# Performance work log

Hardware: AMD Instinct MI355X
Metric: run time of the kernel (lower is better)

## Reference

```python
import jax, jax.numpy as jnp
import numpy as np

N, T, V, C, H = 16, 512, 33, 3, 64
EPS = 1e-5
CONNECTIONS = [(0,1),(1,2),(2,3),(3,7),(0,4),(4,5),(5,6),(6,8),(9,10),(11,12),(11,13),(13,15),(12,14),(14,16),(15,17),(15,19),(15,21),(17,19),(16,18),(16,20),(16,22),(18,20),(11,23),(12,24),(23,24),(23,25),(25,27),(24,26),(26,28),(27,29),(27,31),(29,31),(28,30),(28,32)]


def _adjacency():
    A = np.zeros((V, V), dtype=np.float32)
    for i, j in CONNECTIONS:
        A[i, j] = 1.0
        A[j, i] = 1.0
    A = A + np.eye(V, dtype=np.float32)
    return jnp.asarray(A / A.sum(axis=1, keepdims=True))  # D^{-1} A row-normalization


def setup_inputs() -> dict:
    key = jax.random.key(0)
    ks = iter(jax.random.split(key, 80))
    def nrm(shape, s=0.05):
        return jax.random.normal(next(ks), shape, jnp.float32) * s
    d = {"x": jax.random.normal(next(ks), (N, T, V, C), jnp.float32), "A": _adjacency()}
    def bn(prefix, shape):
        d[prefix + "g"] = 1.0 + nrm(shape, 0.1)
        d[prefix + "b"] = nrm(shape, 0.1)
        d[prefix + "m"] = jnp.zeros(shape, jnp.float32)
        d[prefix + "v"] = jnp.ones(shape, jnp.float32)
    bn("dbn_", (C * V,))
    d["b1_gw"] = nrm((H, C)); d["b1_gb"] = nrm((H,))
    bn("b1_bn1", (H,)); d["b1_tw"] = nrm((H, H, 9)); d["b1_tb"] = nrm((H,)); bn("b1_bn2", (H,))
    d["m_gw"] = nrm((3, H, H)); d["m_gb"] = nrm((3, H))
    bn("m_bn1", (3, H)); d["m_tw"] = nrm((3, H, H, 9)); d["m_tb"] = nrm((3, H)); bn("m_bn2", (3, H))
    d["b5_gw"] = nrm((C, H)); d["b5_gb"] = nrm((C,))
    bn("b5_bn1", (C,)); d["b5_tw"] = nrm((C, C, 9)); d["b5_tb"] = nrm((C,)); bn("b5_bn2", (C,))
    return d


def _bn2d(y, g, b, m, v):
    sh = (1, -1, 1, 1)
    return (y - m.reshape(sh)) * (g.reshape(sh) * jax.lax.rsqrt(v.reshape(sh) + EPS)) + b.reshape(sh)


def _block(y, A, gw, gb, g1, b1, m1, v1, tw, tb, g2, b2, m2, v2, residual):
    res = y if residual else 0.0
    # GraphConv: 1x1 conv (K=1 partition) then joint aggregation with normalized adjacency
    z = jnp.einsum('nctv,oc->notv', y, gw) + gb.reshape(1, -1, 1, 1)
    z = jnp.einsum('nctv,vw->nctw', z, A)
    # TCN: BN -> ReLU -> 9x1 temporal conv (pad 4) -> BN (dropout identity in eval)
    z = jax.nn.relu(_bn2d(z, g1, b1, m1, v1))
    z = jax.lax.conv_general_dilated(z, tw[..., None], (1, 1), [(4, 4), (0, 0)],
                                     dimension_numbers=('NCHW', 'OIHW', 'NCHW')) + tb.reshape(1, -1, 1, 1)
    z = _bn2d(z, g2, b2, m2, v2)
    return jax.nn.relu(z + res)


def _forward(x, A, dbn_g, dbn_b, dbn_m, dbn_v, b1_gw, b1_gb, b1_bn1g, b1_bn1b, b1_bn1m, b1_bn1v, b1_tw, b1_tb, b1_bn2g, b1_bn2b, b1_bn2m, b1_bn2v, m_gw, m_gb, m_bn1g, m_bn1b, m_bn1m, m_bn1v, m_tw, m_tb, m_bn2g, m_bn2b, m_bn2m, m_bn2v, b5_gw, b5_gb, b5_bn1g, b5_bn1b, b5_bn1m, b5_bn1v, b5_tw, b5_tb, b5_bn2g, b5_bn2b, b5_bn2m, b5_bn2v):
    xc = jnp.transpose(x, (0, 3, 1, 2))  # N,C,T,V
    # data_bn: raw view of NCTV contiguous buffer as (N, C*V, T), matching torch .view
    xr = xc.reshape(N, C * V, T)
    xr = (xr - dbn_m[:, None]) * (dbn_g[:, None] * jax.lax.rsqrt(dbn_v[:, None] + EPS)) + dbn_b[:, None]
    y = xr.reshape(N, C, T, V)
    y = _block(y, A, b1_gw, b1_gb, b1_bn1g, b1_bn1b, b1_bn1m, b1_bn1v, b1_tw, b1_tb, b1_bn2g, b1_bn2b, b1_bn2m, b1_bn2v, False)
    for i in range(3):
        y = _block(y, A, m_gw[i], m_gb[i], m_bn1g[i], m_bn1b[i], m_bn1m[i], m_bn1v[i], m_tw[i], m_tb[i], m_bn2g[i], m_bn2b[i], m_bn2m[i], m_bn2v[i], True)
    y = _block(y, A, b5_gw, b5_gb, b5_bn1g, b5_bn1b, b5_bn1m, b5_bn1v, b5_tw, b5_tb, b5_bn2g, b5_bn2b, b5_bn2m, b5_bn2v, False)
    return jnp.transpose(xc + y, (0, 2, 3, 1))  # N,T,V,C


def reference(x, A, dbn_g, dbn_b, dbn_m, dbn_v, b1_gw, b1_gb, b1_bn1g, b1_bn1b, b1_bn1m, b1_bn1v, b1_tw, b1_tb, b1_bn2g, b1_bn2b, b1_bn2m, b1_bn2v, m_gw, m_gb, m_bn1g, m_bn1b, m_bn1m, m_bn1v, m_tw, m_tb, m_bn2g, m_bn2b, m_bn2m, m_bn2v, b5_gw, b5_gb, b5_bn1g, b5_bn1b, b5_bn1m, b5_bn1v, b5_tw, b5_tb, b5_bn2g, b5_bn2b, b5_bn2m, b5_bn2v):
    return _forward(x, A, dbn_g, dbn_b, dbn_m, dbn_v, b1_gw, b1_gb, b1_bn1g, b1_bn1b, b1_bn1m, b1_bn1v, b1_tw, b1_tb, b1_bn2g, b1_bn2b, b1_bn2m, b1_bn2v, m_gw, m_gb, m_bn1g, m_bn1b, m_bn1m, m_bn1v, m_tw, m_tb, m_bn2g, m_bn2b, m_bn2m, m_bn2v, b5_gw, b5_gb, b5_bn1g, b5_bn1b, b5_bn1m, b5_bn1v, b5_tw, b5_tb, b5_bn2g, b5_bn2b, b5_bn2m, b5_bn2v)
```

## Files before the change

kernel.cpp:

```cpp
#include <hip/hip_runtime.h>
#include <hip/hip_bf16.h>


constexpr int N_ = 16, T_ = 512, V_ = 33, C_ = 3, H_ = 64;
constexpr float EPS_ = 1e-5f;

typedef __attribute__((ext_vector_type(8))) short short8;
typedef __attribute__((ext_vector_type(4))) float f32x4;

__device__ inline unsigned short f2bf(float f) {
    union { __hip_bfloat16 h; unsigned short u; } cv;
    cv.h = __float2bfloat16(f);
    return cv.u;
}
__device__ inline float bf2f(unsigned short u) {
    union { unsigned short u; __hip_bfloat16 h; } cv;
    cv.u = u;
    return __bfloat162float(cv.h);
}

__global__ __launch_bounds__(256) void k_prep(
    const float* __restrict__ b1_tw, const float* __restrict__ m_tw,
    const float* __restrict__ b1_gw, const float* __restrict__ m_gw,
    const float* __restrict__ Adj,
    unsigned short* __restrict__ wT_bf, unsigned short* __restrict__ gw_bf,
    unsigned short* __restrict__ ATbf, float* __restrict__ colsum,
    float* __restrict__ gwT_b1)
{
    int idx = blockIdx.x * 256 + threadIdx.x;
    if (idx < 147456) {
        int s = idx / 36864, r = idx % 36864;
        int k = r / 4096, o = (r % 4096) / 64, i = r % 64;
        const float* src = (s == 0) ? b1_tw : (m_tw + (size_t)(s - 1) * 36864);
        wT_bf[idx] = f2bf(src[(o * 64 + i) * 9 + k]);
    } else if (idx < 147456 + 12288) {
        int r = idx - 147456;
        gw_bf[r] = f2bf(m_gw[r]);
    } else if (idx < 147456 + 12288 + 3456) {
        int r = idx - 159744;
        int w = r / 72, vv = r % 72;
        ATbf[r] = (w < 33 && vv < 33) ? f2bf(Adj[vv * 33 + w]) : (unsigned short)0;
    } else if (idx < 147456 + 12288 + 3456 + 48) {
        int w = idx - 163200;
        float s = 0.f;
        if (w < 33)
            for (int vv = 0; vv < 33; ++vv) s += Adj[vv * 33 + w];
        colsum[w] = s;
    } else if (idx < 147456 + 12288 + 3456 + 48 + 192) {
        int r = idx - 163248;
        int c = r / 64, o = r % 64;
        gwT_b1[r] = b1_gw[o * 3 + c];
    }
}

__global__ __launch_bounds__(256) void k_stageA_b1(
    const float* __restrict__ x,
    unsigned short* __restrict__ out,
    const float* __restrict__ Adj,
    const float* __restrict__ gwT,
    const float* __restrict__ gb,
    const float* __restrict__ g1, const float* __restrict__ b1,
    const float* __restrict__ m1, const float* __restrict__ v1,
    const float* __restrict__ dg, const float* __restrict__ db,
    const float* __restrict__ dm, const float* __restrict__ dv)
{
    __shared__ float sy[V_ * 4];
    __shared__ float su[V_ * 68];
    __shared__ float sA[V_ * V_];
    __shared__ float sgwT[3 * 64];

    int nt = blockIdx.x;
    int t = nt & (T_ - 1);
    int tid = threadIdx.x;
    const float* src = x + (size_t)nt * (V_ * 3);
    for (int idx = tid; idx < V_ * 3; idx += 256) {
        int v = idx / 3, c = idx % 3;
        int jj = c * V_ + ((t * V_ + v) >> 9);
        float s = dg[jj] * rsqrtf(dv[jj] + EPS_);
        sy[v * 4 + c] = (src[idx] - dm[jj]) * s + db[jj];
    }
    for (int idx = tid; idx < V_ * V_; idx += 256) sA[idx] = Adj[idx];
    for (int idx = tid; idx < 3 * 64; idx += 256) sgwT[idx] = gwT[idx];
    __syncthreads();

    for (int idx = tid; idx < V_ * 16; idx += 256) {
        int v = idx >> 4, oq = idx & 15, o4 = oq * 4;
        float a0 = gb[o4], a1 = gb[o4 + 1], a2 = gb[o4 + 2], a3 = gb[o4 + 3];
#pragma unroll
        for (int c = 0; c < 3; ++c) {
            float yv = sy[v * 4 + c];
            const float4 w4 = *reinterpret_cast<const float4*>(&sgwT[c * 64 + o4]);
            a0 = fmaf(yv, w4.x, a0); a1 = fmaf(yv, w4.y, a1);
            a2 = fmaf(yv, w4.z, a2); a3 = fmaf(yv, w4.w, a3);
        }
        *reinterpret_cast<float4*>(&su[v * 68 + o4]) = make_float4(a0, a1, a2, a3);
    }
    __syncthreads();

    for (int idx = tid; idx < V_ * 16; idx += 256) {
        int w = idx >> 4, oq = idx & 15, o4 = oq * 4;
        float a0 = 0.f, a1 = 0.f, a2 = 0.f, a3 = 0.f;
        for (int v = 0; v < V_; ++v) {
            float av = sA[v * V_ + w];
            const float4 u4 = *reinterpret_cast<const float4*>(&su[v * 68 + o4]);
            a0 = fmaf(av, u4.x, a0); a1 = fmaf(av, u4.y, a1);
            a2 = fmaf(av, u4.z, a2); a3 = fmaf(av, u4.w, a3);
        }
        float acc[4] = {a0, a1, a2, a3};
        unsigned short r4[4];
#pragma unroll
        for (int j = 0; j < 4; ++j) {
            int o = o4 + j;
            float s = g1[o] * rsqrtf(v1[o] + EPS_);
            float tt = b1[o] - m1[o] * s;
            r4[j] = f2bf(fmaxf(fmaf(acc[j], s, tt), 0.f));
        }
        *reinterpret_cast<ushort4*>(&out[(size_t)nt * (V_ * 64) + w * 64 + o4]) =
            *reinterpret_cast<ushort4*>(r4);
    }
}

__global__ __launch_bounds__(256) void k_stageA_mfma(
    const unsigned short* __restrict__ in,
    unsigned short* __restrict__ out,
    const unsigned short* __restrict__ ATbf,
    const float* __restrict__ colsum,
    const unsigned short* __restrict__ gwbf,
    const float* __restrict__ gb,
    const float* __restrict__ g1, const float* __restrict__ b1,
    const float* __restrict__ m1, const float* __restrict__ v1)
{
    __shared__ unsigned short Ys[4 * 48 * 72];
    __shared__ unsigned short UT[64 * 72];
    __shared__ float cs[48];

    int nt0 = blockIdx.x * 4;
    int tid = threadIdx.x;
    int wv = tid >> 6, lane = tid & 63;
    int l15 = lane & 15, lg = lane >> 4;
    int o = wv * 16 + l15;

    short8 atf[3][2];
#pragma unroll
    for (int mf = 0; mf < 3; ++mf)
#pragma unroll
        for (int kk = 0; kk < 2; ++kk)
            atf[mf][kk] = *reinterpret_cast<const short8*>(
                ATbf + (16 * mf + l15) * 72 + kk * 32 + lg * 8);
    short8 gwf[2];
#pragma unroll
    for (int kk = 0; kk < 2; ++kk)
        gwf[kk] = *reinterpret_cast<const short8*>(gwbf + o * 64 + kk * 32 + lg * 8);

    float gbl = gb[o];
    float s1 = g1[o] * rsqrtf(v1[o] + EPS_);
    float c1 = b1[o] - m1[o] * s1;

    for (int idx = tid; idx < 1056; idx += 256) {
        int j = idx / 264, r = idx % 264;
        int v = r >> 3, cc = r & 7;
        *reinterpret_cast<short8*>(&Ys[(j * 48 + v) * 72 + cc * 8]) =
            *reinterpret_cast<const short8*>(in + ((size_t)(nt0 + j) * V_ + v) * 64 + cc * 8);
    }
    for (int idx = tid; idx < 540; idx += 256) {
        int j = idx / 135, r = idx % 135;
        int v = 33 + r / 9, cc = r % 9;
        short8 z = {};
        *reinterpret_cast<short8*>(&Ys[(j * 48 + v) * 72 + cc * 8]) = z;
    }
    for (int idx = tid; idx < 128; idx += 256) {
        int oo = idx >> 1, cc = idx & 1;
        short8 z = {};
        *reinterpret_cast<short8*>(&UT[oo * 72 + 48 + cc * 8]) = z;
    }
    if (tid < 48) cs[tid] = colsum[tid];
    __syncthreads();

    for (int j = 0; j < 4; ++j) {
#pragma unroll
        for (int mf = 0; mf < 3; ++mf) {
            f32x4 au = {};
#pragma unroll
            for (int kk = 0; kk < 2; ++kk) {
                short8 a = *reinterpret_cast<const short8*>(
                    &Ys[(j * 48 + 16 * mf + l15) * 72 + kk * 32 + lg * 8]);
                au = __builtin_amdgcn_mfma_f32_16x16x32_bf16(a, gwf[kk], au, 0, 0, 0);
            }
            unsigned short pk[4];
            pk[0] = f2bf(au[0]); pk[1] = f2bf(au[1]);
            pk[2] = f2bf(au[2]); pk[3] = f2bf(au[3]);
            *reinterpret_cast<ushort4*>(&UT[o * 72 + 16 * mf + lg * 4]) =
                *reinterpret_cast<ushort4*>(pk);
        }
        short8 bu[2];
#pragma unroll
        for (int kk = 0; kk < 2; ++kk)
            bu[kk] = *reinterpret_cast<const short8*>(&UT[o * 72 + kk * 32 + lg * 8]);
#pragma unroll
        for (int mf2 = 0; mf2 < 3; ++mf2) {
            f32x4 az = {};
#pragma unroll
            for (int kk = 0; kk < 2; ++kk)
                az = __builtin_amdgcn_mfma_f32_16x16x32_bf16(atf[mf2][kk], bu[kk], az, 0, 0, 0);
#pragma unroll
            for (int r = 0; r < 4; ++r) {
                int w = 16 * mf2 + lg * 4 + r;
                if (w < 33) {
                    float val = az[r] + gbl * cs[w];
                    float y = fmaxf(val * s1 + c1, 0.f);
                    out[((size_t)(nt0 + j) * V_ + w) * 64 + o] = f2bf(y);
                }
            }
        }
    }
}

template <bool RES>
__global__ __launch_bounds__(256) void k_stageB_mfma(
    const unsigned short* __restrict__ z,
    unsigned short* __restrict__ out,
    const unsigned short* __restrict__ wbf,
    const float* __restrict__ tb,
    const float* __restrict__ g2, const float* __restrict__ b2,
    const float* __restrict__ m2, const float* __restrict__ vv2)
{
    __shared__ unsigned short sa[2][72 * 64];

    int bx = blockIdx.x, v = blockIdx.y, n = blockIdx.z;
    int base_t0 = bx * 256;
    int tid = threadIdx.x;
    int wv = tid >> 6, lane = tid & 63;
    int l15 = lane & 15, lg = lane >> 4;
    int o = wv * 16 + l15;

    short8 bw[18];
#pragma unroll
    for (int k = 0; k < 9; ++k)
#pragma unroll
        for (int c = 0; c < 2; ++c)
            bw[k * 2 + c] = *reinterpret_cast<const short8*>(
                wbf + ((k * 64 + o) * 64) + c * 32 + lg * 8);

    float s2 = g2[o] * rsqrtf(vv2[o] + EPS_);
    float c2 = (tb[o] - m2[o]) * s2 + b2[o];

    short8 stg[3];

#define LOADJ(jj)                                                             \
    {                                                                         \
        int t0l = base_t0 + (jj) * 64;                                        \
        _Pragma("unroll")                                                     \
        for (int it = 0; it < 3; ++it) {                                      \
            int idx = tid + it * 256;                                         \
            if (idx < 576) {                                                  \
                int r = idx >> 3;                                             \
                int tg = t0l - 4 + r;                                         \
                short8 val = {};                                              \
                if (tg >= 0 && tg < T_)                                       \
                    val = *reinterpret_cast<const short8*>(                   \
                        z + ((size_t)(n * T_ + tg) * V_ + v) * 64 +           \
                        (idx & 7) * 8);                                       \
                stg[it] = val;                                                \
            }                                                                 \
        }                                                                     \
    }

#define WRITEJ(pp)                                                            \
    {                                                                         \
        _Pragma("unroll")                                                     \
        for (int it = 0; it < 3; ++it) {                                      \
            int idx = tid + it * 256;                                         \
            if (idx < 576) {                                                  \
                int r = idx >> 3, cc = idx & 7;                               \
                int slot = cc ^ (r & 7);                                      \
                *reinterpret_cast<short8*>(                                   \
                    reinterpret_cast<char*>(&sa[pp][0]) + r * 128 +           \
                    slot * 16) = stg[it];                                     \
            }                                                                 \
        }                                                                     \
    }

    LOADJ(0);
    WRITEJ(0);
    __syncthreads();

    int p = 0;
    for (int j = 0; j < 4; ++j) {
        if (j < 3) LOADJ(j + 1);

        int t0 = base_t0 + j * 64;

        unsigned short res[16];
        if (RES) {
#pragma unroll
            for (int f = 0; f < 4; ++f)
#pragma unroll
                for (int r = 0; r < 4; ++r) {
                    int t = t0 + f * 16 + lg * 4 + r;
                    res[f * 4 + r] =
                        out[((size_t)(n * T_ + t) * V_ + v) * 64 + o];
                }
        }

        f32x4 acc[4] = {};
        for (int k = 0; k < 9; ++k) {
#pragma unroll
            for (int c = 0; c < 2; ++c) {
                short8 b = bw[k * 2 + c];
#pragma unroll
                for (int f = 0; f < 4; ++f) {
                    int r = f * 16 + l15 + k;
                    int slot = (c * 4 + lg) ^ (r & 7);
                    short8 a = *reinterpret_cast<const short8*>(
                        reinterpret_cast<const char*>(&sa[p][0]) + r * 128 + slot * 16);
                    acc[f] = __builtin_amdgcn_mfma_f32_16x16x32_bf16(a, b, acc[f], 0, 0, 0);
                }
            }
        }

#pragma unroll
        for (int f = 0; f < 4; ++f) {
#pragma unroll
            for (int r = 0; r < 4; ++r) {
                int t = t0 + f * 16 + lg * 4 + r;
                size_t addr = ((size_t)(n * T_ + t) * V_ + v) * 64 + o;
                float zz = acc[f][r] * s2 + c2;
                if (RES) zz += bf2f(res[f * 4 + r]);
                out[addr] = f2bf(fmaxf(zz, 0.f));
            }
        }

        if (j < 3) WRITEJ(p ^ 1);
        __syncthreads();
        p ^= 1;
    }
#undef LOADJ
#undef WRITEJ
}

__global__ __launch_bounds__(256) void k_stageA_b5(
    const unsigned short* __restrict__ in,
    float* __restrict__ out,
    const float* __restrict__ Adj,
    const float* __restrict__ gw,
    const float* __restrict__ gb,
    const float* __restrict__ g1, const float* __restrict__ b1,
    const float* __restrict__ m1, const float* __restrict__ v1)
{
    __shared__ float sy[V_ * 64];
    __shared__ float su[V_ * 4];
    __shared__ float sA[V_ * V_];
    int nt = blockIdx.x;
    int tid = threadIdx.x;
    const unsigned short* src = in + (size_t)nt * (V_ * 64);
    for (int idx = tid; idx < 264; idx += 256) {
        short8 val = *reinterpret_cast<const short8*>(src + idx * 8);
#pragma unroll
        for (int e = 0; e < 8; ++e)
            sy[idx * 8 + e] = bf2f((unsigned short)val[e]);
    }
    for (int idx = tid; idx < V_ * V_; idx += 256) sA[idx] = Adj[idx];
    __syncthreads();
    for (int idx = tid; idx < V_ * 3; idx += 256) {
        int v = idx / 3, o = idx % 3;
        float a = gb[o];
        for (int c = 0; c < 64; ++c) a = fmaf(sy[v * 64 + c], gw[o * 64 + c], a);
        su[v * 4 + o] = a;
    }
    __syncthreads();
    for (int idx = tid; idx < V_ * 3; idx += 256) {
        int w = idx / 3, o = idx % 3;
        float a = 0.f;
        for (int vv = 0; vv < V_; ++vv) a = fmaf(su[vv * 4 + o], sA[vv * V_ + w], a);
        float s = g1[o] * rsqrtf(v1[o] + EPS_);
        float zz = (a - m1[o]) * s + b1[o];
        out[(size_t)nt * (V_ * 3) + w * 3 + o] = fmaxf(zz, 0.f);
    }
}

__global__ __launch_bounds__(256) void k_stageB_b5(
    const float* __restrict__ z5,
    const float* __restrict__ x,
    float* __restrict__ out,
    const float* __restrict__ tw,
    const float* __restrict__ tb,
    const float* __restrict__ g2, const float* __restrict__ b2,
    const float* __restrict__ m2, const float* __restrict__ v2)
{
    int idx = blockIdx.x * 256 + threadIdx.x;
    if (idx >= N_ * T_ * V_) return;
    int v = idx % V_;
    int t = (idx / V_) % T_;
    int n = idx / (V_ * T_);
    float acc0 = tb[0], acc1 = tb[1], acc2 = tb[2];
    for (int k = 0; k < 9; ++k) {
        int tg = t + k - 4;
        if (tg < 0 || tg >= T_) continue;
        const float* zp = &z5[((size_t)(n * T_ + tg) * V_ + v) * 3];
        float zi0 = zp[0], zi1 = zp[1], zi2 = zp[2];
        acc0 = fmaf(tw[0 * 9 + k], zi0, acc0);
        acc0 = fmaf(tw[1 * 9 + k], zi1, acc0);
        acc0 = fmaf(tw[2 * 9 + k], zi2, acc0);
        acc1 = fmaf(tw[3 * 9 + k], zi0, acc1);
        acc1 = fmaf(tw[4 * 9 + k], zi1, acc1);
        acc1 = fmaf(tw[5 * 9 + k], zi2, acc1);
        acc2 = fmaf(tw[6 * 9 + k], zi0, acc2);
        acc2 = fmaf(tw[7 * 9 + k], zi1, acc2);
        acc2 = fmaf(tw[8 * 9 + k], zi2, acc2);
    }
    size_t base = (size_t)idx * 3;
    float a[3] = {acc0, acc1, acc2};
#pragma unroll
    for (int oo = 0; oo < 3; ++oo) {
        float s = g2[oo] * rsqrtf(v2[oo] + EPS_);
        float zz = (a[oo] - m2[oo]) * s + b2[oo];
        out[base + oo] = x[base + oo] + fmaxf(zz, 0.f);
    }
}

extern "C" void kernel_launch(void* const* d_in, const int* in_sizes, int n_in,
                              void* d_out, int out_size, void* d_ws, size_t ws_size,
                              hipStream_t stream) {
    int a = 0;
    const float* x      = (const float*)d_in[a++];
    const float* Adj    = (const float*)d_in[a++];
    const float* dbn_g  = (const float*)d_in[a++];
    const float* dbn_b  = (const float*)d_in[a++];
    const float* dbn_m  = (const float*)d_in[a++];
    const float* dbn_v  = (const float*)d_in[a++];
    const float* b1_gw  = (const float*)d_in[a++];
    const float* b1_gb  = (const float*)d_in[a++];
    const float* b1_bn1g = (const float*)d_in[a++];
    const float* b1_bn1b = (const float*)d_in[a++];
    const float* b1_bn1m = (const float*)d_in[a++];
    const float* b1_bn1v = (const float*)d_in[a++];
    const float* b1_tw  = (const float*)d_in[a++];
    const float* b1_tb  = (const float*)d_in[a++];
    const float* b1_bn2g = (const float*)d_in[a++];
    const float* b1_bn2b = (const float*)d_in[a++];
    const float* b1_bn2m = (const float*)d_in[a++];
    const float* b1_bn2v = (const float*)d_in[a++];
    const float* m_gw   = (const float*)d_in[a++];
    const float* m_gb   = (const float*)d_in[a++];
    const float* m_bn1g = (const float*)d_in[a++];
    const float* m_bn1b = (const float*)d_in[a++];
    const float* m_bn1m = (const float*)d_in[a++];
    const float* m_bn1v = (const float*)d_in[a++];
    const float* m_tw   = (const float*)d_in[a++];
    const float* m_tb   = (const float*)d_in[a++];
    const float* m_bn2g = (const float*)d_in[a++];
    const float* m_bn2b = (const float*)d_in[a++];
    const float* m_bn2m = (const float*)d_in[a++];
    const float* m_bn2v = (const float*)d_in[a++];
    const float* b5_gw  = (const float*)d_in[a++];
    const float* b5_gb  = (const float*)d_in[a++];
    const float* b5_bn1g = (const float*)d_in[a++];
    const float* b5_bn1b = (const float*)d_in[a++];
    const float* b5_bn1m = (const float*)d_in[a++];
    const float* b5_bn1v = (const float*)d_in[a++];
    const float* b5_tw  = (const float*)d_in[a++];
    const float* b5_tb  = (const float*)d_in[a++];
    const float* b5_bn2g = (const float*)d_in[a++];
    const float* b5_bn2b = (const float*)d_in[a++];
    const float* b5_bn2m = (const float*)d_in[a++];
    const float* b5_bn2v = (const float*)d_in[a++];

    char* ws = (char*)d_ws;
    const size_t S_BIG_B  = (size_t)N_ * T_ * V_ * 64 * 2;
    const size_t S_SM_B   = (size_t)N_ * T_ * V_ * 3 * 4;
    unsigned short* B0     = (unsigned short*)(ws);
    unsigned short* B1     = (unsigned short*)(ws + S_BIG_B);
    float*          z5     = (float*)(ws + 2 * S_BIG_B + S_SM_B);
    unsigned short* wT_bf  = (unsigned short*)(ws + 2 * S_BIG_B + 2 * S_SM_B);
    unsigned short* gw_bf  = wT_bf + 147456;
    unsigned short* ATbf   = gw_bf + 12288;
    float*          colsum = (float*)(ATbf + 3456);
    float*          gwT_b1 = colsum + 48;

    k_prep<<<(163440 + 255) / 256, 256, 0, stream>>>(
        b1_tw, m_tw, b1_gw, m_gw, Adj, wT_bf, gw_bf, ATbf, colsum, gwT_b1);

    k_stageA_b1<<<N_ * T_, 256, 0, stream>>>(
        x, B1, Adj, gwT_b1, b1_gb, b1_bn1g, b1_bn1b, b1_bn1m, b1_bn1v,
        dbn_g, dbn_b, dbn_m, dbn_v);
    k_stageB_mfma<false><<<dim3(T_ / 256, V_, N_), 256, 0, stream>>>(
        B1, B0, wT_bf, b1_tb, b1_bn2g, b1_bn2b, b1_bn2m, b1_bn2v);

    for (int i = 0; i < 3; ++i) {
        k_stageA_mfma<<<(N_ * T_) / 4, 256, 0, stream>>>(
            B0, B1, ATbf, colsum, gw_bf + i * 4096, m_gb + i * 64,
            m_bn1g + i * 64, m_bn1b + i * 64, m_bn1m + i * 64, m_bn1v + i * 64);
        k_stageB_mfma<true><<<dim3(T_ / 256, V_, N_), 256, 0, stream>>>(
            B1, B0, wT_bf + (1 + i) * 36864, m_tb + i * 64,
            m_bn2g + i * 64, m_bn2b + i * 64, m_bn2m + i * 64, m_bn2v + i * 64);
    }

    k_stageA_b5<<<N_ * T_, 256, 0, stream>>>(
        B0, z5, Adj, b5_gw, b5_gb, b5_bn1g, b5_bn1b, b5_bn1m, b5_bn1v);
    k_stageB_b5<<<(N_ * T_ * V_ + 255) / 256, 256, 0, stream>>>(
        z5, x, (float*)d_out, b5_tw, b5_tb, b5_bn2g, b5_bn2b, b5_bn2m, b5_bn2v);
}
```

Before: 288.9 us.

## Use MFMA for first block's adjacency aggregation, four timesteps per workgroup

Rewrites the first graph-conv stage so each workgroup handles four (n,t) slices. The joint aggregation now runs as bf16 MFMA using the precomputed transposed adjacency, and the bias enters through adjacency column sums. This replaces scalar FMA loops over a shared fp32 adjacency copy and amortises setup across four timesteps. It adds bf16 rounding of the intermediate before aggregation, which may cost some accuracy.

```diff
diff --git a/kernel.cpp b/kernel.cpp
--- a/kernel.cpp
+++ b/kernel.cpp
@@ -56,7 +56,8 @@
 __global__ __launch_bounds__(256) void k_stageA_b1(
     const float* __restrict__ x,
     unsigned short* __restrict__ out,
-    const float* __restrict__ Adj,
+    const unsigned short* __restrict__ ATbf,
+    const float* __restrict__ colsum,
     const float* __restrict__ gwT,
     const float* __restrict__ gb,
     const float* __restrict__ g1, const float* __restrict__ b1,
@@ -64,59 +65,78 @@
     const float* __restrict__ dg, const float* __restrict__ db,
     const float* __restrict__ dm, const float* __restrict__ dv)
 {
-    __shared__ float sy[V_ * 4];
-    __shared__ float su[V_ * 68];
-    __shared__ float sA[V_ * V_];
-    __shared__ float sgwT[3 * 64];
-
-    int nt = blockIdx.x;
-    int t = nt & (T_ - 1);
+    __shared__ float sy[4][V_ * 4];
+    __shared__ unsigned short UT[64 * 72];
+    __shared__ float cs[48];
+
+    int nt0 = blockIdx.x * 4;
     int tid = threadIdx.x;
-    const float* src = x + (size_t)nt * (V_ * 3);
-    for (int idx = tid; idx < V_ * 3; idx += 256) {
-        int v = idx / 3, c = idx % 3;
+    int wv = tid >> 6, lane = tid & 63;
+    int l15 = lane & 15, lg = lane >> 4;
+    int o = wv * 16 + l15;
+
+    short8 atf[3][2];
+#pragma unroll
+    for (int mf = 0; mf < 3; ++mf)
+#pragma unroll
+        for (int kk = 0; kk < 2; ++kk)
+            atf[mf][kk] = *reinterpret_cast<const short8*>(
+                ATbf + (16 * mf + l15) * 72 + kk * 32 + lg * 8);
+
+    float gw0 = gwT[0 * 64 + o], gw1 = gwT[1 * 64 + o], gw2 = gwT[2 * 64 + o];
+    float gbl = gb[o];
+    float s1 = g1[o] * rsqrtf(v1[o] + EPS_);
+    float c1 = b1[o] - m1[o] * s1;
+
+    for (int idx = tid; idx < 4 * V_ * 3; idx += 256) {
+        int j = idx / (V_ * 3), r = idx % (V_ * 3);
+        int v = r / 3, c = r % 3;
+        int nt = nt0 + j;
+        int t = nt & (T_ - 1);
         int jj = c * V_ + ((t * V_ + v) >> 9);
         float s = dg[jj] * rsqrtf(dv[jj] + EPS_);
-        sy[v * 4 + c] = (src[idx] - dm[jj]) * s + db[jj];
-    }
-    for (int idx = tid; idx < V_ * V_; idx += 256) sA[idx] = Adj[idx];
-    for (int idx = tid; idx < 3 * 64; idx += 256) sgwT[idx] = gwT[idx];
+        sy[j][v * 4 + c] = (x[(size_t)nt * (V_ * 3) + r] - dm[jj]) * s + db[jj];
+    }
+    for (int idx = tid; idx < 128; idx += 256) {
+        int oo = idx >> 1, cc = idx & 1;
+        short8 z = {};
+        *reinterpret_cast<short8*>(&UT[oo * 72 + 48 + cc * 8]) = z;
+    }
+    if (tid < 48) cs[tid] = colsum[tid];
     __syncthreads();
 
-    for (int idx = tid; idx < V_ * 16; idx += 256) {
-        int v = idx >> 4, oq = idx & 15, o4 = oq * 4;
-        float a0 = gb[o4], a1 = gb[o4 + 1], a2 = gb[o4 + 2], a3 = gb[o4 + 3];
-#pragma unroll
-        for (int c = 0; c < 3; ++c) {
-            float yv = sy[v * 4 + c];
-            const float4 w4 = *reinterpret_cast<const float4*>(&sgwT[c * 64 + o4]);
-            a0 = fmaf(yv, w4.x, a0); a1 = fmaf(yv, w4.y, a1);
-            a2 = fmaf(yv, w4.z, a2); a3 = fmaf(yv, w4.w, a3);
-        }
-        *reinterpret_cast<float4*>(&su[v * 68 + o4]) = make_float4(a0, a1, a2, a3);
-    }
-    __syncthreads();
-
-    for (int idx = tid; idx < V_ * 16; idx += 256) {
-        int w = idx >> 4, oq = idx & 15, o4 = oq * 4;
-        float a0 = 0.f, a1 = 0.f, a2 = 0.f, a3 = 0.f;
-        for (int v = 0; v < V_; ++v) {
-            float av = sA[v * V_ + w];
-            const float4 u4 = *reinterpret_cast<const float4*>(&su[v * 68 + o4]);
-            a0 = fmaf(av, u4.x, a0); a1 = fmaf(av, u4.y, a1);
-            a2 = fmaf(av, u4.z, a2); a3 = fmaf(av, u4.w, a3);
-        }
-        float acc[4] = {a0, a1, a2, a3};
-        unsigned short r4[4];
-#pragma unroll
-        for (int j = 0; j < 4; ++j) {
-            int o = o4 + j;
-            float s = g1[o] * rsqrtf(v1[o] + EPS_);
-            float tt = b1[o] - m1[o] * s;
-            r4[j] = f2bf(fmaxf(fmaf(acc[j], s, tt), 0.f));
-        }
-        *reinterpret_cast<ushort4*>(&out[(size_t)nt * (V_ * 64) + w * 64 + o4]) =
-            *reinterpret_cast<ushort4*>(r4);
+    for (int j = 0; j < 4; ++j) {
+#pragma unroll
+        for (int it = 0; it < 12; ++it) {
+            int v = lg + it * 4;
+            float u = 0.f;
+            if (v < V_) {
+                u = sy[j][v * 4 + 0] * gw0;
+                u = fmaf(sy[j][v * 4 + 1], gw1, u);
+                u = fmaf(sy[j][v * 4 + 2], gw2, u);
+            }
+            UT[o * 72 + v] = f2bf(u);
+        }
+        short8 bu[2];
+#pragma unroll
+        for (int kk = 0; kk < 2; ++kk)
+            bu[kk] = *reinterpret_cast<const short8*>(&UT[o * 72 + kk * 32 + lg * 8]);
+#pragma unroll
+        for (int mf2 = 0; mf2 < 3; ++mf2) {
+            f32x4 az = {};
+#pragma unroll
+            for (int kk = 0; kk < 2; ++kk)
+                az = __builtin_amdgcn_mfma_f32_16x16x32_bf16(atf[mf2][kk], bu[kk], az, 0, 0, 0);
+#pragma unroll
+            for (int r = 0; r < 4; ++r) {
+                int w = 16 * mf2 + lg * 4 + r;
+                if (w < 33) {
+                    float val = az[r] + gbl * cs[w];
+                    float y = fmaxf(val * s1 + c1, 0.f);
+                    out[((size_t)(nt0 + j) * V_ + w) * 64 + o] = f2bf(y);
+                }
+            }
+        }
     }
 }
 
@@ -480,8 +500,8 @@
     k_prep<<<(163440 + 255) / 256, 256, 0, stream>>>(
         b1_tw, m_tw, b1_gw, m_gw, Adj, wT_bf, gw_bf, ATbf, colsum, gwT_b1);
 
-    k_stageA_b1<<<N_ * T_, 256, 0, stream>>>(
-        x, B1, Adj, gwT_b1, b1_gb, b1_bn1g, b1_bn1b, b1_bn1m, b1_bn1v,
+    k_stageA_b1<<<(N_ * T_) / 4, 256, 0, stream>>>(
+        x, B1, ATbf, colsum, gwT_b1, b1_gb, b1_bn1g, b1_bn1b, b1_bn1m, b1_bn1v,
         dbn_g, dbn_b, dbn_m, dbn_v);
     k_stageB_mfma<false><<<dim3(T_ / 256, V_, N_), 256, 0, stream>>>(
         B1, B0, wT_bf, b1_tb, b1_bn2g, b1_bn2b, b1_bn2m, b1_bn2v);
```

Result: faster. 270.3 us (-6.4%).
